# Kernel optimization log

Hardware: AMD Instinct MI355X
Metric: run time of the kernel (lower is better)

Reference implementation:

```python
import jax, jax.numpy as jnp
import numpy as np

B, S, E, H = 2, 2048, 1024, 16
D = E // H
NORM = np.float32(np.sqrt(E))


def setup_inputs() -> dict:
    key = jax.random.key(0)
    ks = jax.random.split(key, 5)
    scale = np.float32(E ** -0.5)
    x = jax.random.normal(ks[0], (B, S, E), jnp.float32)
    Wq = jax.random.normal(ks[1], (E, E), jnp.float32) * scale
    Wk = jax.random.normal(ks[2], (E, E), jnp.float32) * scale
    Wv = jax.random.normal(ks[3], (E, E), jnp.float32) * scale
    Wo = jax.random.normal(ks[4], (E, E), jnp.float32) * scale
    return {"encoded_vectors": x, "Wq": Wq, "Wk": Wk, "Wv": Wv, "Wo": Wo}


def reference(encoded_vectors, Wq, Wk, Wv, Wo):
    x = encoded_vectors                      # [B,S,E]
    q = x @ Wq.T                             # nn.Linear(bias=False): x @ W^T
    k = x @ Wk.T
    v = x @ Wv.T
    skip_val = v                             # residual is the v-projection output
    qh = q.reshape(B, S, H, D).transpose(0, 2, 1, 3)  # [B,H,S,D]
    kh = k.reshape(B, S, H, D).transpose(0, 2, 1, 3)
    vh = v.reshape(B, S, H, D).transpose(0, 2, 1, 3)
    scores = jnp.einsum('bhsd,bhtd->bhst', qh, kh)    # [B,H,S,S]
    # causal additive mask: -inf strictly above the diagonal (triu, k=1)
    mask = jnp.triu(jnp.full((S, S), -jnp.inf, jnp.float32), 1)
    logits = (scores + mask) / NORM          # mask added BEFORE scaling, per source
    p = jax.nn.softmax(logits, axis=-1)
    # faithful to torch.einsum('stuu,stuv->stuv'): diagonal of p scales v elementwise
    attn = jnp.einsum('bhss,bhsd->bhsd', p, vh)       # [B,H,S,D]
    out = attn.transpose(0, 2, 1, 3).reshape(B, S, E)
    return out @ Wo.T + skip_val
```

## Files before the change

kernel.cpp:

```cpp
#include <hip/hip_runtime.h>
#include <hip/hip_bf16.h>

#define B_ 2
#define S_ 2048
#define E_ 1024
#define H_ 16
#define D_ 64
#define M_ (B_*S_)

typedef unsigned short u16;
typedef __attribute__((ext_vector_type(8))) short short8;
typedef __attribute__((ext_vector_type(4))) short short4v;
typedef __attribute__((ext_vector_type(4))) float f32x4;

__device__ __forceinline__ float b2f(u16 u) {
    union { float f; unsigned int i; } x; x.i = ((unsigned int)u) << 16; return x.f;
}
__device__ __forceinline__ u16 f2b(float f) {
    union { float f; unsigned int i; } x; x.f = f;
    unsigned int r = x.i + 0x7fffu + ((x.i >> 16) & 1u);
    return (u16)(r >> 16);
}

#if __has_builtin(__builtin_amdgcn_exp2f)
__device__ __forceinline__ float ex2(float x) { return __builtin_amdgcn_exp2f(x); }
#else
__device__ __forceinline__ float ex2(float x) {
    float r; asm("v_exp_f32 %0, %1" : "=v"(r) : "v"(x)); return r;
}
#endif

__global__ __launch_bounds__(256)
void cvt_kernel(const float* __restrict__ X,
                const float* __restrict__ Wq, const float* __restrict__ Wk,
                const float* __restrict__ Wv, const float* __restrict__ Wo,
                u16* __restrict__ Xb, u16* __restrict__ Wqb, u16* __restrict__ Wkb,
                u16* __restrict__ Wvb, u16* __restrict__ Wob,
                float* __restrict__ lsum)
{
    int bid = blockIdx.x;
    if (bid >= 8192) {
        size_t i4 = (size_t)(bid - 8192) * 256 + threadIdx.x;
        ((float4*)lsum)[i4] = make_float4(0.f, 0.f, 0.f, 0.f);
        return;
    }
    const float* src; u16* dst; int blk;
    if (bid < 4096) { src = X; dst = Xb; blk = bid; }
    else {
        int w = (bid - 4096) >> 10;
        blk = (bid - 4096) & 1023;
        src = (w == 0) ? Wq : (w == 1) ? Wk : (w == 2) ? Wv : Wo;
        dst = (w == 0) ? Wqb : (w == 1) ? Wkb : (w == 2) ? Wvb : Wob;
    }
    size_t i4 = (size_t)blk * 256 + threadIdx.x;
    float4 v = ((const float4*)src)[i4];
    short4v o;
    o.x = (short)f2b(v.x); o.y = (short)f2b(v.y);
    o.z = (short)f2b(v.z); o.w = (short)f2b(v.w);
    *(short4v*)(dst + i4 * 4) = o;
}

#define BN 128
#define BK 64

template<int ROWS>
__device__ __forceinline__ void stage64(const u16* __restrict__ gbase, u16* lds,
                                        int ldg, int wave, int lane)
{
    constexpr int ITERS = ROWS * 8 / 256;
    #pragma unroll
    for (int n = 0; n < ITERS; ++n) {
        int q = (wave * ITERS + n) * 64 + lane;
        int r = q >> 3, slot = q & 7;
        int c = slot ^ ((r >> 1) & 7);
        const u16* g = gbase + (size_t)r * ldg + c * 8;
        u16* l = lds + (size_t)(wave * ITERS + n) * 512;
        __builtin_amdgcn_global_load_lds(
            (const __attribute__((address_space(1))) unsigned int*)g,
            (__attribute__((address_space(3))) unsigned int*)l, 16, 0, 0);
    }
}

template<int BMT>
__device__ __forceinline__ void gemm_bt_acc(
    const u16* __restrict__ A, const u16* __restrict__ Bm,
    int Kd, int bm, int bn, f32x4 (*acc)[4])
{
    constexpr int NI = BMT / 32;
    __shared__ u16 lA[BMT * BK];
    __shared__ u16 lB[BN * BK];
    const int tid  = threadIdx.x;
    const int wave = tid >> 6, lane = tid & 63;
    const int quad = lane >> 4, l16 = lane & 15;
    const int wm = (wave & 1) * (BMT / 2), wn = (wave >> 1) * 64;

    for (int k0 = 0; k0 < Kd; k0 += BK) {
        stage64<BMT>(A  + (size_t)bm * Kd + k0, lA, Kd, wave, lane);
        stage64<BN>(Bm + (size_t)bn * Kd + k0, lB, Kd, wave, lane);
        __syncthreads();
        #pragma unroll
        for (int s = 0; s < 2; ++s) {
            short8 af[NI], bf[4];
            #pragma unroll
            for (int i = 0; i < NI; ++i) {
                int R = wm + i * 16 + l16;
                int sc = s * 4 + quad;
                af[i] = *(const short8*)&lA[R * 64 + ((sc ^ ((R >> 1) & 7)) * 8)];
            }
            #pragma unroll
            for (int j = 0; j < 4; ++j) {
                int R = wn + j * 16 + l16;
                int sc = s * 4 + quad;
                bf[j] = *(const short8*)&lB[R * 64 + ((sc ^ ((R >> 1) & 7)) * 8)];
            }
            #pragma unroll
            for (int i = 0; i < NI; ++i)
                #pragma unroll
                for (int j = 0; j < 4; ++j)
                    acc[i][j] = __builtin_amdgcn_mfma_f32_16x16x32_bf16(af[i], bf[j], acc[i][j], 0, 0, 0);
        }
        __syncthreads();
    }
}

__global__ __launch_bounds__(256, 3)
void qkv_kernel(const u16* __restrict__ X,
                const u16* __restrict__ Wq, const u16* __restrict__ Wk, const u16* __restrict__ Wv,
                u16* __restrict__ Q, u16* __restrict__ K, u16* __restrict__ V)
{
    const u16* W = (blockIdx.z == 0) ? Wq : (blockIdx.z == 1) ? Wk : Wv;
    u16* C = (blockIdx.z == 0) ? Q : (blockIdx.z == 1) ? K : V;
    const int bm = blockIdx.x * 128, bn = blockIdx.y * BN;
    f32x4 acc[4][4];
    #pragma unroll
    for (int i = 0; i < 4; ++i)
        #pragma unroll
        for (int j = 0; j < 4; ++j) acc[i][j] = (f32x4){0.f,0.f,0.f,0.f};
    gemm_bt_acc<128>(X, W, E_, bm, bn, acc);

    const int wave = threadIdx.x >> 6, lane = threadIdx.x & 63;
    const int quad = lane >> 4, l16 = lane & 15;
    const int wm = (wave & 1) * 64, wn = (wave >> 1) * 64;
    #pragma unroll
    for (int i = 0; i < 4; ++i)
        #pragma unroll
        for (int j = 0; j < 4; ++j) {
            int row0 = bm + wm + i * 16 + quad * 4;
            int col  = bn + wn + j * 16 + l16;
            #pragma unroll
            for (int r = 0; r < 4; ++r)
                C[(size_t)(row0 + r) * E_ + col] = f2b(acc[i][j][r]);
        }
}

__global__ __launch_bounds__(256, 4)
void out_kernel(const u16* __restrict__ An, const u16* __restrict__ Wo,
                const u16* __restrict__ V, float* __restrict__ Out)
{
    const int bm = blockIdx.x * 64, bn = blockIdx.y * BN;
    f32x4 acc[2][4];
    #pragma unroll
    for (int i = 0; i < 2; ++i)
        #pragma unroll
        for (int j = 0; j < 4; ++j) acc[i][j] = (f32x4){0.f,0.f,0.f,0.f};
    gemm_bt_acc<64>(An, Wo, E_, bm, bn, acc);

    const int wave = threadIdx.x >> 6, lane = threadIdx.x & 63;
    const int quad = lane >> 4, l16 = lane & 15;
    const int wm = (wave & 1) * 32, wn = (wave >> 1) * 64;
    #pragma unroll
    for (int i = 0; i < 2; ++i)
        #pragma unroll
        for (int j = 0; j < 4; ++j) {
            int row0 = bm + wm + i * 16 + quad * 4;
            int col  = bn + wn + j * 16 + l16;
            #pragma unroll
            for (int r = 0; r < 4; ++r) {
                size_t idx = (size_t)(row0 + r) * E_ + col;
                Out[idx] = acc[i][j][r] + b2f(V[idx]);
            }
        }
}

__global__ __launch_bounds__(256, 4)
void attn_tiles_kernel(const u16* __restrict__ Q, const u16* __restrict__ Kp,
                       float* __restrict__ lsum, float* __restrict__ ed)
{
    __shared__ u16 lK[128 * 64];
    const int tau = blockIdx.x;
    const int bh  = blockIdx.y;
    const int b = bh >> 4, h = bh & 15;
    int ii = 0;
    while ((ii + 1) * (ii + 2) / 2 <= tau) ++ii;
    const int jj = tau - ii * (ii + 1) / 2;
    const bool diag = (ii == jj);
    const int wave = threadIdx.x >> 6, lane = threadIdx.x & 63;
    const int quad = lane >> 4, l16 = lane & 15;
    const float CE = 0.04508422002778f;

    const u16* kg = Kp + ((size_t)(b * S_) + jj * 128) * E_ + h * D_;
    #pragma unroll
    for (int m4 = 0; m4 < 4; ++m4) {
        int q = m4 * 256 + wave * 64 + lane;
        int slot = q & 3, hr = q >> 2;
        int f = hr >> 7, r = hr & 127;
        int c = f * 4 + (slot ^ ((r >> 1) & 3));
        const u16* g = kg + (size_t)r * E_ + c * 8;
        u16* l = lK + (size_t)(m4 * 256 + wave * 64) * 8;
        __builtin_amdgcn_global_load_lds(
            (const __attribute__((address_space(1))) unsigned int*)g,
            (__attribute__((address_space(3))) unsigned int*)l, 16, 0, 0);
    }

    short8 aq[2][2];
    #pragma unroll
    for (int m = 0; m < 2; ++m) {
        const u16* qp = Q + ((size_t)(b * S_) + ii * 128 + wave * 32 + m * 16 + l16) * E_
                        + h * D_ + quad * 8;
        aq[m][0] = *(const short8*)qp;
        aq[m][1] = *(const short8*)(qp + 32);
    }
    __syncthreads();

    f32x4 acc[2][8];
    #pragma unroll
    for (int m = 0; m < 2; ++m)
        #pragma unroll
        for (int n = 0; n < 8; ++n) acc[m][n] = (f32x4){0.f,0.f,0.f,0.f};

    #pragma unroll
    for (int nt = 0; nt < 8; ++nt) {
        int R = nt * 16 + l16;
        int sw = (R >> 1) & 3;
        short8 bk0 = *(const short8*)&lK[((0 * 128 + R) * 4 + (quad ^ sw)) * 8];
        short8 bk1 = *(const short8*)&lK[((1 * 128 + R) * 4 + (quad ^ sw)) * 8];
        #pragma unroll
        for (int m = 0; m < 2; ++m) {
            acc[m][nt] = __builtin_amdgcn_mfma_f32_16x16x32_bf16(aq[m][0], bk0, acc[m][nt], 0, 0, 0);
            acc[m][nt] = __builtin_amdgcn_mfma_f32_16x16x32_bf16(aq[m][1], bk1, acc[m][nt], 0, 0, 0);
        }
    }

    float rs[2][4];
    #pragma unroll
    for (int m = 0; m < 2; ++m)
        #pragma unroll
        for (int r = 0; r < 4; ++r) rs[m][r] = 0.f;

    #pragma unroll
    for (int m = 0; m < 2; ++m)
        #pragma unroll
        for (int nt = 0; nt < 8; ++nt)
            #pragma unroll
            for (int r = 0; r < 4; ++r) {
                float e = ex2(acc[m][nt][r] * CE);
                if (diag) {
                    int srow = wave * 32 + m * 16 + quad * 4 + r;
                    int tcol = nt * 16 + l16;
                    if (tcol > srow) e = 0.f;
                    if (tcol == srow)
                        ed[(size_t)bh * S_ + ii * 128 + srow] = e;
                }
                rs[m][r] += e;
            }

    #pragma unroll
    for (int m = 0; m < 2; ++m)
        #pragma unroll
        for (int r = 0; r < 4; ++r) {
            float v = rs[m][r];
            v += __shfl_xor(v, 1); v += __shfl_xor(v, 2);
            v += __shfl_xor(v, 4); v += __shfl_xor(v, 8);
            if (l16 == 0) {
                int srow = ii * 128 + wave * 32 + m * 16 + quad * 4 + r;
                atomicAdd(&lsum[(size_t)bh * S_ + srow], v);
            }
        }
}

__global__ __launch_bounds__(256)
void scale_v_kernel(const u16* __restrict__ V, const float* __restrict__ lsum,
                    const float* __restrict__ ed, u16* __restrict__ An)
{
    size_t i = (size_t)blockIdx.x * blockDim.x + threadIdx.x;
    size_t base = i * 8;
    int e = (int)(base & (E_ - 1));
    size_t bs = base >> 10;
    int h = e >> 6;
    int b = (int)(bs >> 11);
    int s = (int)(bs & (S_ - 1));
    size_t li = ((size_t)(b * H_ + h)) * S_ + s;
    float p = ed[li] / lsum[li];
    int4 pk = *(const int4*)(V + base);
    u16* u = (u16*)&pk;
    #pragma unroll
    for (int j = 0; j < 8; ++j) u[j] = f2b(b2f(u[j]) * p);
    *(int4*)(An + base) = pk;
}

extern "C" void kernel_launch(void* const* d_in, const int* in_sizes, int n_in,
                              void* d_out, int out_size, void* d_ws, size_t ws_size,
                              hipStream_t stream)
{
    const float* X  = (const float*)d_in[0];
    const float* Wq = (const float*)d_in[1];
    const float* Wk = (const float*)d_in[2];
    const float* Wv = (const float*)d_in[3];
    const float* Wo = (const float*)d_in[4];
    float* Out = (float*)d_out;

    u16* Xb  = (u16*)d_ws;
    u16* Wqb = Xb  + (size_t)M_ * E_;
    u16* Wkb = Wqb + (size_t)E_ * E_;
    u16* Wvb = Wkb + (size_t)E_ * E_;
    u16* Wob = Wvb + (size_t)E_ * E_;
    u16* Q   = Wob + (size_t)E_ * E_;
    u16* K   = Q   + (size_t)M_ * E_;
    u16* V   = K   + (size_t)M_ * E_;
    u16* An  = V   + (size_t)M_ * E_;
    float* lsum = (float*)(An + (size_t)M_ * E_);
    float* ed   = lsum + (size_t)B_ * H_ * S_;

    cvt_kernel<<<dim3(8192 + 64), dim3(256), 0, stream>>>(X, Wq, Wk, Wv, Wo,
                                                          Xb, Wqb, Wkb, Wvb, Wob, lsum);
    qkv_kernel<<<dim3(M_/128, E_/BN, 3), dim3(256), 0, stream>>>(Xb, Wqb, Wkb, Wvb, Q, K, V);
    attn_tiles_kernel<<<dim3(136, B_*H_), dim3(256), 0, stream>>>(Q, K, lsum, ed);
    scale_v_kernel<<<dim3((M_*E_/8)/256), dim3(256), 0, stream>>>(V, lsum, ed, An);
    out_kernel<<<dim3(M_/64, E_/BN), dim3(256), 0, stream>>>(An, Wob, V, Out);
}
```

Measured before the change: 153.2 us.

## Fuse softmax-diagonal V scaling into output projection GEMM A-tile staging

Removes the separate scale_v kernel and its intermediate An buffer. The out_kernel now computes per-row p = ed/lsum into shared memory and scales V while staging the A tile into LDS. This saves one launch and a full write/read of an M×E bf16 tensor. In exchange, the scaling is recomputed for every N-block, and A staging goes through registers instead of the shared gemm helper.

```diff
diff --git a/kernel.cpp b/kernel.cpp
--- a/kernel.cpp
+++ b/kernel.cpp
@@ -154,20 +154,75 @@
 }
 
 __global__ __launch_bounds__(256, 4)
-void out_kernel(const u16* __restrict__ An, const u16* __restrict__ Wo,
-                const u16* __restrict__ V, float* __restrict__ Out)
-{
+void out_kernel(const u16* __restrict__ V, const u16* __restrict__ Wo,
+                const float* __restrict__ lsum, const float* __restrict__ ed,
+                float* __restrict__ Out)
+{
+    __shared__ u16 lA[64 * BK];
+    __shared__ u16 lB[BN * BK];
+    __shared__ float lp[H_ * 64];
     const int bm = blockIdx.x * 64, bn = blockIdx.y * BN;
-    f32x4 acc[2][4];
-    #pragma unroll
-    for (int i = 0; i < 2; ++i)
-        #pragma unroll
-        for (int j = 0; j < 4; ++j) acc[i][j] = (f32x4){0.f,0.f,0.f,0.f};
-    gemm_bt_acc<64>(An, Wo, E_, bm, bn, acc);
-
-    const int wave = threadIdx.x >> 6, lane = threadIdx.x & 63;
+    const int tid  = threadIdx.x;
+    const int wave = tid >> 6, lane = tid & 63;
     const int quad = lane >> 4, l16 = lane & 15;
     const int wm = (wave & 1) * 32, wn = (wave >> 1) * 64;
+    const int bb = bm >> 11, sbase = bm & (S_ - 1);
+
+    #pragma unroll
+    for (int n = 0; n < 4; ++n) {
+        int idx = n * 256 + tid;
+        int h = idx >> 6, r = idx & 63;
+        size_t li = ((size_t)(bb * H_ + h)) * S_ + sbase + r;
+        lp[idx] = ed[li] / lsum[li];
+    }
+    __syncthreads();
+
+    f32x4 acc[2][4];
+    #pragma unroll
+    for (int i = 0; i < 2; ++i)
+        #pragma unroll
+        for (int j = 0; j < 4; ++j) acc[i][j] = (f32x4){0.f,0.f,0.f,0.f};
+
+    for (int k0 = 0; k0 < E_; k0 += BK) {
+        const int h = k0 >> 6;
+        stage64<BN>(Wo + (size_t)bn * E_ + k0, lB, E_, wave, lane);
+        #pragma unroll
+        for (int n = 0; n < 2; ++n) {
+            int q = n * 256 + tid;
+            int r = q >> 3, slot = q & 7;
+            int c = slot ^ ((r >> 1) & 7);
+            float p = lp[h * 64 + r];
+            int4 pk = *(const int4*)(V + (size_t)(bm + r) * E_ + k0 + c * 8);
+            u16* u = (u16*)&pk;
+            #pragma unroll
+            for (int jq = 0; jq < 8; ++jq) u[jq] = f2b(b2f(u[jq]) * p);
+            *(int4*)(lA + (size_t)q * 8) = pk;
+        }
+        __syncthreads();
+        #pragma unroll
+        for (int s = 0; s < 2; ++s) {
+            short8 af[2], bf[4];
+            #pragma unroll
+            for (int i = 0; i < 2; ++i) {
+                int R = wm + i * 16 + l16;
+                int sc = s * 4 + quad;
+                af[i] = *(const short8*)&lA[R * 64 + ((sc ^ ((R >> 1) & 7)) * 8)];
+            }
+            #pragma unroll
+            for (int j = 0; j < 4; ++j) {
+                int R = wn + j * 16 + l16;
+                int sc = s * 4 + quad;
+                bf[j] = *(const short8*)&lB[R * 64 + ((sc ^ ((R >> 1) & 7)) * 8)];
+            }
+            #pragma unroll
+            for (int i = 0; i < 2; ++i)
+                #pragma unroll
+                for (int j = 0; j < 4; ++j)
+                    acc[i][j] = __builtin_amdgcn_mfma_f32_16x16x32_bf16(af[i], bf[j], acc[i][j], 0, 0, 0);
+        }
+        __syncthreads();
+    }
+
     #pragma unroll
     for (int i = 0; i < 2; ++i)
         #pragma unroll
@@ -278,26 +333,6 @@
         }
 }
 
-__global__ __launch_bounds__(256)
-void scale_v_kernel(const u16* __restrict__ V, const float* __restrict__ lsum,
-                    const float* __restrict__ ed, u16* __restrict__ An)
-{
-    size_t i = (size_t)blockIdx.x * blockDim.x + threadIdx.x;
-    size_t base = i * 8;
-    int e = (int)(base & (E_ - 1));
-    size_t bs = base >> 10;
-    int h = e >> 6;
-    int b = (int)(bs >> 11);
-    int s = (int)(bs & (S_ - 1));
-    size_t li = ((size_t)(b * H_ + h)) * S_ + s;
-    float p = ed[li] / lsum[li];
-    int4 pk = *(const int4*)(V + base);
-    u16* u = (u16*)&pk;
-    #pragma unroll
-    for (int j = 0; j < 8; ++j) u[j] = f2b(b2f(u[j]) * p);
-    *(int4*)(An + base) = pk;
-}
-
 extern "C" void kernel_launch(void* const* d_in, const int* in_sizes, int n_in,
                               void* d_out, int out_size, void* d_ws, size_t ws_size,
                               hipStream_t stream)
@@ -317,14 +352,12 @@
     u16* Q   = Wob + (size_t)E_ * E_;
     u16* K   = Q   + (size_t)M_ * E_;
     u16* V   = K   + (size_t)M_ * E_;
-    u16* An  = V   + (size_t)M_ * E_;
-    float* lsum = (float*)(An + (size_t)M_ * E_);
+    float* lsum = (float*)(V + (size_t)M_ * E_);
     float* ed   = lsum + (size_t)B_ * H_ * S_;
 
     cvt_kernel<<<dim3(8192 + 64), dim3(256), 0, stream>>>(X, Wq, Wk, Wv, Wo,
                                                           Xb, Wqb, Wkb, Wvb, Wob, lsum);
     qkv_kernel<<<dim3(M_/128, E_/BN, 3), dim3(256), 0, stream>>>(Xb, Wqb, Wkb, Wvb, Q, K, V);
     attn_tiles_kernel<<<dim3(136, B_*H_), dim3(256), 0, stream>>>(Q, K, lsum, ed);
-    scale_v_kernel<<<dim3((M_*E_/8)/256), dim3(256), 0, stream>>>(V, lsum, ed, An);
-    out_kernel<<<dim3(M_/64, E_/BN), dim3(256), 0, stream>>>(An, Wob, V, Out);
-}
+    out_kernel<<<dim3(M_/64, E_/BN), dim3(256), 0, stream>>>(V, Wob, lsum, ed, Out);
+}
```

After: 156.2 us. About the same (+1.9%).
